# Kernel tuning notes

Measured on AMD Instinct MI355X. Metric: run time of the kernel, lower is better.

Reference implementation:

```python
import jax, jax.numpy as jnp
import numpy as np

MARGIN = 0.3
N, D = 8192, 128
NUM_CLASSES = 512


def setup_inputs() -> dict:
    key = jax.random.key(0)
    k1, k2 = jax.random.split(key)
    embeddings = jax.random.normal(k1, (N, D), dtype=jnp.float32)
    targets = jax.random.randint(k2, (N,), 0, NUM_CLASSES, dtype=jnp.int64)
    return {"embeddings": embeddings, "targets": targets}


def reference(embeddings, targets):
    x = embeddings.astype(jnp.float32)
    # pairwise squared-euclidean: ||xi||^2 + ||xj||^2 - 2 xi.xj, clamped then sqrt
    sq = jnp.sum(x * x, axis=1)  # [N]
    dist = sq[:, None] + sq[None, :] - 2.0 * (x @ x.T)
    dist = jnp.sqrt(jnp.clip(dist, 1e-12, None))  # [N, N]

    is_pos = targets[:, None] == targets[None, :]  # includes diagonal, as in torch code

    # batch-hard mining: per-row hardest positive (max) and hardest negative (min)
    dist_ap = jnp.max(jnp.where(is_pos, dist, -jnp.inf), axis=1)
    dist_an = jnp.min(jnp.where(is_pos, jnp.inf, dist), axis=1)

    # MarginRankingLoss(margin)(dist_an, dist_ap, y=1) = mean(relu(margin - (dist_an - dist_ap)))
    loss = jnp.mean(jax.nn.relu(dist_ap - dist_an + MARGIN))
    return loss
```

## Files before the change

### kernel.cpp

```cpp
#include <hip/hip_runtime.h>
#include <hip/hip_bf16.h>

#define N_ROWS 8192
#define DIM 128
#define MARGIN_F 0.3f

typedef __attribute__((ext_vector_type(8))) short short8;
typedef __attribute__((ext_vector_type(4))) float f32x4;

__global__ __launch_bounds__(256) void prep_kernel(
    const float* __restrict__ x, const int* __restrict__ tgt,
    unsigned short* __restrict__ xbA, unsigned short* __restrict__ xbB,
    float2* __restrict__ meta, int* __restrict__ apb, int* __restrict__ anb,
    unsigned long long* __restrict__ lsum, unsigned int* __restrict__ lcnt) {
  if (blockIdx.x == 0 && threadIdx.x == 0) { *lsum = 0ull; *lcnt = 0u; }
  const int w = threadIdx.x >> 6, l = threadIdx.x & 63;
  const int row = blockIdx.x * 4 + w;
  float2 v = reinterpret_cast<const float2*>(x + (size_t)row * DIM)[l];
  __hip_bfloat16 b0 = __float2bfloat16(v.x);
  __hip_bfloat16 b1 = __float2bfloat16(v.y);
  __hip_bfloat16 a0 = __float2bfloat16(-2.f * v.x);
  __hip_bfloat16 a1 = __float2bfloat16(-2.f * v.y);
  ushort2 stB, stA;
  stB.x = *reinterpret_cast<unsigned short*>(&b0);
  stB.y = *reinterpret_cast<unsigned short*>(&b1);
  stA.x = *reinterpret_cast<unsigned short*>(&a0);
  stA.y = *reinterpret_cast<unsigned short*>(&a1);
  const int c16 = row >> 4, l15r = row & 15;
  const int unit = c16 * 256 + (l >> 4) * 64 + ((l >> 2) & 3) * 16 + l15r;
  reinterpret_cast<ushort2*>(xbB)[unit * 4 + (l & 3)] = stB;
  reinterpret_cast<ushort2*>(xbA)[unit * 4 + (l & 3)] = stA;

  float s = v.x * v.x + v.y * v.y;
  #pragma unroll
  for (int off = 32; off >= 1; off >>= 1) s += __shfl_xor(s, off);
  if (l == 0) {
    float2 m;
    m.x = s;
    m.y = __int_as_float(tgt[row]);
    meta[row] = m;
    apb[row] = 0x00000000;
    anb[row] = 0x7f800000;
  }
}

__global__ __launch_bounds__(256, 2) void gram_mine_kernel(
    const unsigned short* __restrict__ xbA, const unsigned short* __restrict__ xbB,
    const float2* __restrict__ meta, int* __restrict__ apb, int* __restrict__ anb) {
  const int t = threadIdx.x;
  const int w = t >> 6, l = t & 63;
  const int l15 = l & 15, l4 = l >> 4;
  const int rb = blockIdx.x * 128 + w * 32;
  const int cu = blockIdx.y * 1024;
  const int cv = cu + 512;

  const short8* xfA = reinterpret_cast<const short8*>(xbA);
  const short8* xfB = reinterpret_cast<const short8*>(xbB);

  short8 a0[4], a1[4];
  #pragma unroll
  for (int kk = 0; kk < 4; ++kk) {
    a0[kk] = xfA[(rb >> 4) * 256 + kk * 64 + l];
    a1[kk] = xfA[((rb >> 4) + 1) * 256 + kk * 64 + l];
  }

  int t_r[8];
  #pragma unroll
  for (int rf = 0; rf < 2; ++rf)
    #pragma unroll
    for (int rg = 0; rg < 4; ++rg)
      t_r[rf * 4 + rg] = __float_as_int(meta[rb + rf * 16 + l4 * 4 + rg].y);

  float ap2[8], an2[8];
  #pragma unroll
  for (int i = 0; i < 8; ++i) { ap2[i] = -__builtin_inff(); an2[i] = __builtin_inff(); }

  short8 bu[8], bv[8];
  float2 mu0[2], mu1[2], mv0[2], mv1[2];
  f32x4 accu[2][2], accv[2][2];

#define PREF(BASE, IDX, BB, MC) do {                                          \
    const int cb16_ = ((BASE) >> 4) + (IDX) * 2;                              \
    _Pragma("unroll")                                                         \
    for (int kk_ = 0; kk_ < 4; ++kk_) {                                       \
      BB[kk_ * 2 + 0] = xfB[(cb16_ + 0) * 256 + kk_ * 64 + l];                \
      BB[kk_ * 2 + 1] = xfB[(cb16_ + 1) * 256 + kk_ * 64 + l];                \
    }                                                                         \
    MC[0] = meta[(BASE) + (IDX) * 32 + l15];                                  \
    MC[1] = meta[(BASE) + (IDX) * 32 + 16 + l15]; } while (0)

#define MFMA_T(BB, MC, ACC) do {                                              \
    _Pragma("unroll")                                                         \
    for (int cf_ = 0; cf_ < 2; ++cf_) {                                       \
      float s_ = MC[cf_].x;                                                   \
      f32x4 ci_ = {s_, s_, s_, s_};                                           \
      ACC[0][cf_] = ci_; ACC[1][cf_] = ci_;                                   \
    }                                                                         \
    __builtin_amdgcn_s_setprio(1);                                            \
    _Pragma("unroll")                                                         \
    for (int kk_ = 0; kk_ < 4; ++kk_) {                                       \
      _Pragma("unroll")                                                       \
      for (int cf_ = 0; cf_ < 2; ++cf_) {                                     \
        ACC[0][cf_] = __builtin_amdgcn_mfma_f32_16x16x32_bf16(                \
            a0[kk_], BB[kk_ * 2 + cf_], ACC[0][cf_], 0, 0, 0);                \
        ACC[1][cf_] = __builtin_amdgcn_mfma_f32_16x16x32_bf16(                \
            a1[kk_], BB[kk_ * 2 + cf_], ACC[1][cf_], 0, 0, 0);                \
      } }                                                                     \
    __builtin_amdgcn_s_setprio(0); } while (0)

#define EPI_T(ACC, MC) do {                                                   \
    _Pragma("unroll")                                                         \
    for (int cf_ = 0; cf_ < 2; ++cf_) {                                       \
      const int tc_ = __float_as_int(MC[cf_].y);                              \
      _Pragma("unroll")                                                       \
      for (int rf_ = 0; rf_ < 2; ++rf_) {                                     \
        _Pragma("unroll")                                                     \
        for (int rg_ = 0; rg_ < 4; ++rg_) {                                   \
          const int ix_ = rf_ * 4 + rg_;                                      \
          float v_ = ACC[rf_][cf_][rg_];                                      \
          bool p_ = (t_r[ix_] == tc_);                                        \
          ap2[ix_] = p_ ? fmaxf(ap2[ix_], v_) : ap2[ix_];                     \
          an2[ix_] = p_ ? an2[ix_] : fminf(an2[ix_], v_);                     \
        } } } } while (0)

  PREF(cu, 0, bu, mu0);
  PREF(cv, 0, bv, mv0);

  #pragma unroll 1
  for (int q = 0; q < 8; ++q) {
    const int te = 2 * q;
    const int n1 = te + 1;
    const int n2 = (te + 2 < 16) ? te + 2 : 15;
    MFMA_T(bu, mu0, accu); PREF(cu, n1, bu, mu1);
    MFMA_T(bv, mv0, accv); PREF(cv, n1, bv, mv1);
    EPI_T(accu, mu0); EPI_T(accv, mv0);
    MFMA_T(bu, mu1, accu); PREF(cu, n2, bu, mu0);
    MFMA_T(bv, mv1, accv); PREF(cv, n2, bv, mv0);
    EPI_T(accu, mu1); EPI_T(accv, mv1);
  }

#undef PREF
#undef MFMA_T
#undef EPI_T

  #pragma unroll
  for (int i = 0; i < 8; ++i) {
    #pragma unroll
    for (int off = 1; off < 16; off <<= 1) {
      ap2[i] = fmaxf(ap2[i], __shfl_xor(ap2[i], off));
      an2[i] = fminf(an2[i], __shfl_xor(an2[i], off));
    }
  }
  if (l15 == 0) {
    #pragma unroll
    for (int rf = 0; rf < 2; ++rf)
      #pragma unroll
      for (int rg = 0; rg < 4; ++rg) {
        int row = rb + rf * 16 + l4 * 4 + rg;
        float sqr = meta[row].x;
        float a2 = fmaxf(ap2[rf * 4 + rg] + sqr, 1e-12f);
        float n2 = fmaxf(an2[rf * 4 + rg] + sqr, 1e-12f);
        atomicMax(apb + row, __float_as_int(a2));
        atomicMin(anb + row, __float_as_int(n2));
      }
  }
}

__global__ __launch_bounds__(1024) void loss_kernel(
    const int* __restrict__ apb, const int* __restrict__ anb,
    unsigned long long* __restrict__ lsum, unsigned int* __restrict__ lcnt,
    float* __restrict__ out) {
  __shared__ float red[16];
  const int i = blockIdx.x * 1024 + threadIdx.x;
  float ap = sqrtf(__int_as_float(apb[i]));
  float an = sqrtf(__int_as_float(anb[i]));
  float li = ap - an + MARGIN_F;
  float s = li > 0.f ? li : 0.f;
  #pragma unroll
  for (int off = 32; off >= 1; off >>= 1) s += __shfl_xor(s, off);
  const int w = threadIdx.x >> 6, l = threadIdx.x & 63;
  if (l == 0) red[w] = s;
  __syncthreads();
  if (threadIdx.x < 16) {
    float v = red[threadIdx.x];
    #pragma unroll
    for (int off = 8; off >= 1; off >>= 1) v += __shfl_xor(v, off);
    if (threadIdx.x == 0) {
      unsigned long long q = (unsigned long long)(long long)((double)v * 4194304.0);
      atomicAdd(lsum, q);
      __threadfence();
      unsigned int old = atomicAdd(lcnt, 1u);
      if (old == gridDim.x - 1) {
        unsigned long long tot = atomicAdd(lsum, 0ull);
        out[0] = (float)((double)tot * (1.0 / 4194304.0) / (double)N_ROWS);
      }
    }
  }
}

extern "C" void kernel_launch(void* const* d_in, const int* in_sizes, int n_in,
                              void* d_out, int out_size, void* d_ws, size_t ws_size,
                              hipStream_t stream) {
  const float* x = (const float*)d_in[0];
  const int* tgt = (const int*)d_in[1];
  float* out = (float*)d_out;

  char* ws = (char*)d_ws;
  unsigned short* xbA = (unsigned short*)ws;
  unsigned short* xbB = (unsigned short*)(ws + 2097152);
  float2* meta = (float2*)(ws + 4194304);
  int* apb = (int*)(ws + 4259840);
  int* anb = (int*)(ws + 4292608);
  unsigned long long* lsum = (unsigned long long*)(ws + 4325376);
  unsigned int* lcnt = (unsigned int*)(ws + 4325384);

  prep_kernel<<<2048, 256, 0, stream>>>(x, tgt, xbA, xbB, meta, apb, anb, lsum, lcnt);
  gram_mine_kernel<<<dim3(64, 8), 256, 0, stream>>>(xbA, xbB, meta, apb, anb);
  loss_kernel<<<8, 1024, 0, stream>>>(apb, anb, lsum, lcnt, out);
}
```

Baseline: 47.54 us.

## Split column range into more blocks and drop manual double-buffered prefetch

Each block now handles 256 columns instead of 1024, so the grid grows fourfold (64x32 blocks), and launch bounds now ask for 4 blocks per CU. The hand-written software pipeline that interleaved two column streams with register prefetch is replaced by a simple fully unrolled loop over 8 column tiles. The aim is to raise occupancy and parallelism so that latency hiding comes from more waves rather than explicit prefetch. The cost is more atomic updates to the per-row min/max buffers, reloading the A fragments in every block, and tighter register limits.

```diff
diff --git a/kernel.cpp b/kernel.cpp
--- a/kernel.cpp
+++ b/kernel.cpp
@@ -44,15 +44,15 @@
   }
 }
 
-__global__ __launch_bounds__(256, 2) void gram_mine_kernel(
+__global__ __launch_bounds__(256, 4) void gram_mine_kernel(
     const unsigned short* __restrict__ xbA, const unsigned short* __restrict__ xbB,
     const float2* __restrict__ meta, int* __restrict__ apb, int* __restrict__ anb) {
   const int t = threadIdx.x;
   const int w = t >> 6, l = t & 63;
   const int l15 = l & 15, l4 = l >> 4;
   const int rb = blockIdx.x * 128 + w * 32;
-  const int cu = blockIdx.y * 1024;
-  const int cv = cu + 512;
+  const int chunk = blockIdx.y * 256;
+  const int chunkb = chunk >> 4;
 
   const short8* xfA = reinterpret_cast<const short8*>(xbA);
   const short8* xfB = reinterpret_cast<const short8*>(xbB);
@@ -75,73 +75,55 @@
   #pragma unroll
   for (int i = 0; i < 8; ++i) { ap2[i] = -__builtin_inff(); an2[i] = __builtin_inff(); }
 
-  short8 bu[8], bv[8];
-  float2 mu0[2], mu1[2], mv0[2], mv1[2];
-  f32x4 accu[2][2], accv[2][2];
-
-#define PREF(BASE, IDX, BB, MC) do {                                          \
-    const int cb16_ = ((BASE) >> 4) + (IDX) * 2;                              \
-    _Pragma("unroll")                                                         \
-    for (int kk_ = 0; kk_ < 4; ++kk_) {                                       \
-      BB[kk_ * 2 + 0] = xfB[(cb16_ + 0) * 256 + kk_ * 64 + l];                \
-      BB[kk_ * 2 + 1] = xfB[(cb16_ + 1) * 256 + kk_ * 64 + l];                \
-    }                                                                         \
-    MC[0] = meta[(BASE) + (IDX) * 32 + l15];                                  \
-    MC[1] = meta[(BASE) + (IDX) * 32 + 16 + l15]; } while (0)
-
-#define MFMA_T(BB, MC, ACC) do {                                              \
-    _Pragma("unroll")                                                         \
-    for (int cf_ = 0; cf_ < 2; ++cf_) {                                       \
-      float s_ = MC[cf_].x;                                                   \
-      f32x4 ci_ = {s_, s_, s_, s_};                                           \
-      ACC[0][cf_] = ci_; ACC[1][cf_] = ci_;                                   \
-    }                                                                         \
-    __builtin_amdgcn_s_setprio(1);                                            \
-    _Pragma("unroll")                                                         \
-    for (int kk_ = 0; kk_ < 4; ++kk_) {                                       \
-      _Pragma("unroll")                                                       \
-      for (int cf_ = 0; cf_ < 2; ++cf_) {                                     \
-        ACC[0][cf_] = __builtin_amdgcn_mfma_f32_16x16x32_bf16(                \
-            a0[kk_], BB[kk_ * 2 + cf_], ACC[0][cf_], 0, 0, 0);                \
-        ACC[1][cf_] = __builtin_amdgcn_mfma_f32_16x16x32_bf16(                \
-            a1[kk_], BB[kk_ * 2 + cf_], ACC[1][cf_], 0, 0, 0);                \
-      } }                                                                     \
-    __builtin_amdgcn_s_setprio(0); } while (0)
-
-#define EPI_T(ACC, MC) do {                                                   \
-    _Pragma("unroll")                                                         \
-    for (int cf_ = 0; cf_ < 2; ++cf_) {                                       \
-      const int tc_ = __float_as_int(MC[cf_].y);                              \
-      _Pragma("unroll")                                                       \
-      for (int rf_ = 0; rf_ < 2; ++rf_) {                                     \
-        _Pragma("unroll")                                                     \
-        for (int rg_ = 0; rg_ < 4; ++rg_) {                                   \
-          const int ix_ = rf_ * 4 + rg_;                                      \
-          float v_ = ACC[rf_][cf_][rg_];                                      \
-          bool p_ = (t_r[ix_] == tc_);                                        \
-          ap2[ix_] = p_ ? fmaxf(ap2[ix_], v_) : ap2[ix_];                     \
-          an2[ix_] = p_ ? an2[ix_] : fminf(an2[ix_], v_);                     \
-        } } } } while (0)
-
-  PREF(cu, 0, bu, mu0);
-  PREF(cv, 0, bv, mv0);
-
-  #pragma unroll 1
-  for (int q = 0; q < 8; ++q) {
-    const int te = 2 * q;
-    const int n1 = te + 1;
-    const int n2 = (te + 2 < 16) ? te + 2 : 15;
-    MFMA_T(bu, mu0, accu); PREF(cu, n1, bu, mu1);
-    MFMA_T(bv, mv0, accv); PREF(cv, n1, bv, mv1);
-    EPI_T(accu, mu0); EPI_T(accv, mv0);
-    MFMA_T(bu, mu1, accu); PREF(cu, n2, bu, mu0);
-    MFMA_T(bv, mv1, accv); PREF(cv, n2, bv, mv0);
-    EPI_T(accu, mu1); EPI_T(accv, mv1);
-  }
-
-#undef PREF
-#undef MFMA_T
-#undef EPI_T
+  #pragma unroll
+  for (int ct = 0; ct < 8; ++ct) {
+    const int cb16 = chunkb + ct * 2;
+
+    short8 b[8];
+    #pragma unroll
+    for (int kk = 0; kk < 4; ++kk) {
+      b[kk * 2 + 0] = xfB[(cb16 + 0) * 256 + kk * 64 + l];
+      b[kk * 2 + 1] = xfB[(cb16 + 1) * 256 + kk * 64 + l];
+    }
+    float2 mc0 = meta[chunk + ct * 32 + l15];
+    float2 mc1 = meta[chunk + ct * 32 + 16 + l15];
+
+    f32x4 acc[2][2];
+    {
+      f32x4 c0 = {mc0.x, mc0.x, mc0.x, mc0.x};
+      f32x4 c1 = {mc1.x, mc1.x, mc1.x, mc1.x};
+      acc[0][0] = c0; acc[1][0] = c0;
+      acc[0][1] = c1; acc[1][1] = c1;
+    }
+
+    __builtin_amdgcn_s_setprio(1);
+    #pragma unroll
+    for (int kk = 0; kk < 4; ++kk) {
+      #pragma unroll
+      for (int cf = 0; cf < 2; ++cf) {
+        acc[0][cf] = __builtin_amdgcn_mfma_f32_16x16x32_bf16(
+            a0[kk], b[kk * 2 + cf], acc[0][cf], 0, 0, 0);
+        acc[1][cf] = __builtin_amdgcn_mfma_f32_16x16x32_bf16(
+            a1[kk], b[kk * 2 + cf], acc[1][cf], 0, 0, 0);
+      }
+    }
+    __builtin_amdgcn_s_setprio(0);
+
+    #pragma unroll
+    for (int cf = 0; cf < 2; ++cf) {
+      const int tc = __float_as_int(cf == 0 ? mc0.y : mc1.y);
+      #pragma unroll
+      for (int rf = 0; rf < 2; ++rf)
+        #pragma unroll
+        for (int rg = 0; rg < 4; ++rg) {
+          const int ix = rf * 4 + rg;
+          float v = acc[rf][cf][rg];
+          bool p = (t_r[ix] == tc);
+          ap2[ix] = p ? fmaxf(ap2[ix], v) : ap2[ix];
+          an2[ix] = p ? an2[ix] : fminf(an2[ix], v);
+        }
+    }
+  }
 
   #pragma unroll
   for (int i = 0; i < 8; ++i) {
@@ -215,6 +197,6 @@
   unsigned int* lcnt = (unsigned int*)(ws + 4325384);
 
   prep_kernel<<<2048, 256, 0, stream>>>(x, tgt, xbA, xbB, meta, apb, anb, lsum, lcnt);
-  gram_mine_kernel<<<dim3(64, 8), 256, 0, stream>>>(xbA, xbB, meta, apb, anb);
+  gram_mine_kernel<<<dim3(64, 32), 256, 0, stream>>>(xbA, xbB, meta, apb, anb);
   loss_kernel<<<8, 1024, 0, stream>>>(apb, anb, lsum, lcnt, out);
 }
```

Result: faster. 46.55 us (-2.1%).
